# Performance work log

Measured on AMD Instinct MI355X. Metric: run time of the kernel, lower is better.

## Reference

```python
import jax, jax.numpy as jnp
import numpy as np

PAD_token, SOS_token, EOS_token = 0, 1, 2
V, E, H, B, To, Ti = 10000, 512, 512, 32, 256, 1024


def _u(key, shape, fan_in):
    s = 1.0 / np.sqrt(fan_in)
    return jax.random.uniform(key, shape, jnp.float32, -s, s)


def setup_inputs() -> dict:
    key = jax.random.key(0)
    ks = jax.random.split(key, 16)
    inp = {
        "padded_input": jax.random.randint(ks[0], (B, To), 3, V),
        "encoder_padded_outputs": jax.random.normal(ks[1], (B, Ti, H), jnp.float32),
        "embedding": jax.random.normal(ks[2], (V, E), jnp.float32) * 0.02,
        # layer 0 LSTMCell: input = embed + encoder context (E + H)
        "Wih0": _u(ks[3], (4 * H, E + H), H), "Whh0": _u(ks[4], (4 * H, H), H),
        "bih0": _u(ks[5], (4 * H,), H),       "bhh0": _u(ks[6], (4 * H,), H),
        # layer 1 LSTMCell: input = H
        "Wih1": _u(ks[7], (4 * H, H), H),     "Whh1": _u(ks[8], (4 * H, H), H),
        "bih1": _u(ks[9], (4 * H,), H),       "bhh1": _u(ks[10], (4 * H,), H),
        # MLP: Linear(2H -> H), Tanh, Linear(H -> V)
        "W1": _u(ks[11], (H, 2 * H), 2 * H),  "b1": _u(ks[12], (H,), 2 * H),
        "W2": _u(ks[13], (V, H), H),          "b2": _u(ks[14], (V,), H),
    }
    return inp


def _lstm_cell(x, h, c, Wih, Whh, bih, bhh):
    g = x @ Wih.T + bih + h @ Whh.T + bhh            # [B, 4H]
    i, f, gg, o = jnp.split(g, 4, axis=-1)           # torch gate order i,f,g,o
    c2 = jax.nn.sigmoid(f) * c + jax.nn.sigmoid(i) * jnp.tanh(gg)
    h2 = jax.nn.sigmoid(o) * jnp.tanh(c2)
    return h2, c2


def reference(padded_input, encoder_padded_outputs, embedding,
              Wih0, Whh0, bih0, bhh0, Wih1, Whh1, bih1, bhh1,
              W1, b1, W2, b2):
    n = padded_input.shape[0]
    sos = jnp.full((n, 1), SOS_token, padded_input.dtype)
    eos = jnp.full((n, 1), EOS_token, padded_input.dtype)
    ys_in = jnp.concatenate([sos, padded_input], axis=1)   # [B, To+1]
    ys_out = jnp.concatenate([padded_input, eos], axis=1)  # [B, To+1]

    emb = embedding[ys_in]                                 # [B, To+1, E]
    emb_t = jnp.swapaxes(emb, 0, 1)                        # [To+1, B, E]
    enc = encoder_padded_outputs                           # [B, Ti, H]

    h0 = jnp.zeros((n, H), enc.dtype)
    init = (h0, h0, h0, h0, jnp.zeros((n, enc.shape[2]), enc.dtype))

    def step(carry, e_t):
        h_0, c_0, h_1, c_1, att_c = carry
        rnn_in = jnp.concatenate([e_t, att_c], axis=1)
        h_0, c_0 = _lstm_cell(rnn_in, h_0, c_0, Wih0, Whh0, bih0, bhh0)
        h_1, c_1 = _lstm_cell(h_0, h_1, c_1, Wih1, Whh1, bih1, bhh1)
        scores = jnp.einsum('bh,bth->bt', h_1, enc)        # [B, Ti]
        att_w = jax.nn.softmax(scores, axis=-1)
        att_c = jnp.einsum('bt,bth->bh', att_w, enc)       # [B, H]
        mlp_in = jnp.concatenate([h_1, att_c], axis=1)
        logits = jnp.tanh(mlp_in @ W1.T + b1) @ W2.T + b2  # [B, V]
        return (h_0, c_0, h_1, c_1, att_c), logits

    _, y_all = jax.lax.scan(step, init, emb_t)             # [To+1, B, V]
    logits = jnp.swapaxes(y_all, 0, 1).reshape(-1, V)      # [B*(To+1), V]
    labels = ys_out.reshape(-1)
    logp = jax.nn.log_softmax(logits, axis=-1)
    nll = -jnp.take_along_axis(logp, labels[:, None], axis=1)[:, 0]
    mask = (labels != PAD_token).astype(logits.dtype)
    loss = jnp.sum(nll * mask) / jnp.maximum(jnp.sum(mask), 1.0)
    return loss
```

## Files before the change

### kernel.cpp

```cpp
#include <hip/hip_runtime.h>
#include <hip/hip_bf16.h>

#define B_    32
#define TO_   256
#define T_    257
#define H_    512
#define V_    10000
#define TI_   1024
#define NROW_ 8224
#define NB_   256

using f32x4 = __attribute__((ext_vector_type(4))) float;
using s16x8 = __attribute__((ext_vector_type(8))) short;

struct Ptrs {
  const int* padded;
  const float* enc;
  const float* emb;
  const float *Wih0, *Whh0, *bih0, *bhh0;
  const float *Wih1, *Whh1, *bih1, *bhh1;
  const float *W1, *b1, *W2, *b2;
  float* out;
  unsigned short *mlpin;
  unsigned short *embt;
  unsigned short *tanhv;
  unsigned short *W0c;
  unsigned short *W1c;
  unsigned short *W1b;
  unsigned short *W2b;
  float *bias0c, *bias1c;
  float *u;
  unsigned short *Xh0;
  unsigned short *Xh1;
  float *Xh1f;
  float *Zb;
  unsigned *bar;
  float *rowsum;
  float *lablog;
};

__device__ __forceinline__ unsigned short f2b(float f){
  __hip_bfloat16 h = __float2bfloat16(f);
  unsigned short r; __builtin_memcpy(&r, &h, 2); return r;
}
__device__ __forceinline__ float b2f(unsigned short u){
  unsigned v = ((unsigned)u) << 16; float f; __builtin_memcpy(&f, &v, 4); return f;
}
__device__ __forceinline__ float sigf(float x){ return 1.f / (1.f + expf(-x)); }

__device__ __forceinline__ float aldf(const float* p){
  return __hip_atomic_load(p, __ATOMIC_RELAXED, __HIP_MEMORY_SCOPE_AGENT);
}
__device__ __forceinline__ unsigned long long aldu(const unsigned long long* p){
  return __hip_atomic_load(p, __ATOMIC_RELAXED, __HIP_MEMORY_SCOPE_AGENT);
}
__device__ __forceinline__ void astf(float* p, float v){
  __hip_atomic_store(p, v, __ATOMIC_RELAXED, __HIP_MEMORY_SCOPE_AGENT);
}
__device__ __forceinline__ void astu(unsigned long long* p, unsigned long long v){
  __hip_atomic_store(p, v, __ATOMIC_RELAXED, __HIP_MEMORY_SCOPE_AGENT);
}
__device__ __forceinline__ void astw(unsigned* p, unsigned v){
  __hip_atomic_store(p, v, __ATOMIC_RELAXED, __HIP_MEMORY_SCOPE_AGENT);
}

__device__ __forceinline__ void gbar(unsigned* bar, unsigned ph){
  asm volatile("s_waitcnt vmcnt(0)" ::: "memory");
  __syncthreads();
  if (threadIdx.x == 0){
    const int g = (int)(blockIdx.x >> 5);
    unsigned a = __hip_atomic_fetch_add(bar + g * 64, 1u, __ATOMIC_RELAXED, __HIP_MEMORY_SCOPE_AGENT);
    bool done = false;
    if (a == 31u){
      unsigned r = __hip_atomic_fetch_add(bar + 512, 1u, __ATOMIC_RELAXED, __HIP_MEMORY_SCOPE_AGENT);
      if (r == 7u){
        __hip_atomic_store(bar + 512, 0u, __ATOMIC_RELAXED, __HIP_MEMORY_SCOPE_AGENT);
        #pragma unroll
        for (int i = 0; i < 8; ++i)
          __hip_atomic_store(bar + i * 64, 0u, __ATOMIC_RELAXED, __HIP_MEMORY_SCOPE_AGENT);
        asm volatile("s_waitcnt vmcnt(0)" ::: "memory");
        #pragma unroll
        for (int i = 0; i < 8; ++i)
          __hip_atomic_store(bar + (16 + i) * 64, ph, __ATOMIC_RELAXED, __HIP_MEMORY_SCOPE_AGENT);
        done = true;
      }
    }
    if (!done){
      while (__hip_atomic_load(bar + (16 + g) * 64, __ATOMIC_RELAXED, __HIP_MEMORY_SCOPE_AGENT) != ph)
        __builtin_amdgcn_s_sleep(2);
    }
  }
  __syncthreads();
}

__global__ __launch_bounds__(256) void kprep(Ptrs P){
  const int stride = gridDim.x * blockDim.x;
  const int i0 = blockIdx.x * blockDim.x + threadIdx.x;
  for (int i = i0; i < 2048; i += stride) P.bar[i] = 0u;
  for (int i = i0; i < T_ * B_ * 512; i += stride){
    int k = i & 511, tb = i >> 9, b = tb & 31, t = tb >> 5;
    int tok = (t == 0) ? 1 : P.padded[b * TO_ + (t - 1)];
    P.embt[i] = f2b(P.emb[(size_t)tok * 512 + k]);
  }
  for (int i = i0; i < 2048 * 1536; i += stride){
    int k = i % 1536, gp = i / 1536;
    int j = gp >> 2, q = gp & 3, g = q * 512 + j;
    float v = (k < 1024) ? P.Wih0[(size_t)g * 1024 + k] : P.Whh0[(size_t)g * 512 + (k - 1024)];
    P.W0c[i] = f2b(v);
  }
  for (int i = i0; i < 2048 * 1024; i += stride){
    int k = i & 1023, gp = i >> 10;
    int j = gp >> 2, q = gp & 3, g = q * 512 + j;
    float v = (k < 512) ? P.Wih1[(size_t)g * 512 + k] : P.Whh1[(size_t)g * 512 + (k - 512)];
    P.W1c[i] = f2b(v);
  }
  for (int i = i0; i < 2048; i += stride){
    int j = i >> 2, q = i & 3, g = q * 512 + j;
    P.bias0c[i] = P.bih0[g] + P.bhh0[g];
    P.bias1c[i] = P.bih1[g] + P.bhh1[g];
  }
  for (int i = i0; i < 512 * 1024; i += stride) P.W1b[i] = f2b(P.W1[i]);
  for (int i = i0; i < NROW_; i += stride) P.rowsum[i] = 0.f;
}

__global__ __launch_bounds__(256) void kprep2(Ptrs P){
  const int stride = gridDim.x * blockDim.x;
  const int i0 = blockIdx.x * blockDim.x + threadIdx.x;
  for (int i = i0; i < V_ * 512; i += stride) P.W2b[i] = f2b(P.W2[i]);
}

__global__ __launch_bounds__(256, 1) void kA(Ptrs P){
  __shared__ __align__(16) unsigned short enc_s[128 * 512];
  __shared__ float h1_s[512];
  __shared__ float w_s[128];
  __shared__ float gate_s[32][17];
  __shared__ float h_s[32][4];
  const int bb = blockIdx.x, tid = threadIdx.x;
  const int b_att = bb >> 3;
  unsigned ph = 0;

  {
    const float* ep = P.enc + ((size_t)b_att * TI_ + (size_t)(bb & 7) * 128) * H_;
    for (int idx = tid; idx < 128 * 512; idx += 256){
      int r = idx >> 9;
      unsigned byteoff = ((unsigned)idx * 2u) ^ ((unsigned)(r & 7) << 4);
      enc_s[byteoff >> 1] = f2b(ep[idx]);
    }
  }
  {
    int g = bb * 256 + tid;
    if (g < 32768){ astf(P.u + g, 0.f); astf(P.Xh1f + g, 0.f); }
    if (g < 16384){ astw((unsigned*)P.Xh0 + g, 0u); astw((unsigned*)P.Xh1 + g, 0u); }
    if (g < 64) astf(P.Zb + g, (g >= 32) ? 1.f : 0.f);
  }
  gbar(P.bar, ++ph);

  const int wv = tid >> 6;
  const int l  = tid & 63, lr = l & 15, lk = l >> 4;
  const int eidx = tid - 128;
  const int eb = eidx >> 2, ejl = eidx & 3;
  float c0r = 0.f, c1r = 0.f;

  for (int t = 0; t < T_; ++t){
    const int p = t & 1, pp = p ^ 1;
    if (bb < 128){
      if (wv < 2){
        const int batch = wv * 16 + lr;
        const unsigned short* Brow = P.W0c + (size_t)(bb * 16 + lr) * 1536;
        const unsigned short* Erow = P.embt + ((size_t)t * 32 + batch) * 512;
        const float* Urow = P.u + pp * 16384 + batch * 512;
        const unsigned long long* Hrow =
            (const unsigned long long*)(P.Xh0 + pp * 16384 + batch * 512);
        const float rZ = 1.f / aldf(P.Zb + pp * 32 + batch);
        f32x4 acc = {0.f, 0.f, 0.f, 0.f};
        #pragma unroll
        for (int ks = 0; ks < 16; ++ks){
          s16x8 a = *(const s16x8*)(Erow + ks * 32 + lk * 8);
          s16x8 b = *(const s16x8*)(Brow + ks * 32 + lk * 8);
          acc = __builtin_amdgcn_mfma_f32_16x16x32_bf16(a, b, acc, 0, 0, 0);
        }
        #pragma unroll
        for (int ks = 0; ks < 16; ++ks){
          const int kb = ks * 32 + lk * 8;
          unsigned long long dd[4];
          dd[0] = aldu((const unsigned long long*)(Urow + kb));
          dd[1] = aldu((const unsigned long long*)(Urow + kb + 2));
          dd[2] = aldu((const unsigned long long*)(Urow + kb + 4));
          dd[3] = aldu((const unsigned long long*)(Urow + kb + 6));
          float uf[8]; __builtin_memcpy(uf, dd, 32);
          s16x8 a;
          #pragma unroll
          for (int e = 0; e < 8; ++e) a[e] = (short)f2b(uf[e] * rZ);
          s16x8 b = *(const s16x8*)(Brow + 512 + kb);
          acc = __builtin_amdgcn_mfma_f32_16x16x32_bf16(a, b, acc, 0, 0, 0);
        }
        #pragma unroll
        for (int ks = 0; ks < 16; ++ks){
          const int kb = ks * 32 + lk * 8;
          unsigned long long dd[2];
          dd[0] = aldu(Hrow + (kb >> 2));
          dd[1] = aldu(Hrow + (kb >> 2) + 1);
          s16x8 a; __builtin_memcpy(&a, dd, 16);
          s16x8 b = *(const s16x8*)(Brow + 1024 + kb);
          acc = __builtin_amdgcn_mfma_f32_16x16x32_bf16(a, b, acc, 0, 0, 0);
        }
        #pragma unroll
        for (int j = 0; j < 4; ++j) gate_s[wv * 16 + lk * 4 + j][lr] = acc[j];
      }
    } else if (bb < 160 && t > 0){
      const int b = bb - 128;
      const float rZ = 1.f / aldf(P.Zb + pp * 32 + b);
      unsigned long long v = aldu((const unsigned long long*)(P.u + pp * 16384 + b * 512) + tid);
      float f2[2]; __builtin_memcpy(f2, &v, 8);
      unsigned pk = (unsigned)f2b(f2[0] * rZ) | ((unsigned)f2b(f2[1] * rZ) << 16);
      *(unsigned*)(P.mlpin + ((size_t)(t - 1) * 32 + b) * 1024 + 512 + tid * 2) = pk;
    }
    __syncthreads();
    if (bb < 128 && tid >= 128){
      const float* bs = P.bias0c + bb * 16 + ejl * 4;
      float ii = sigf (gate_s[eb][ejl * 4 + 0] + bs[0]);
      float ff = sigf (gate_s[eb][ejl * 4 + 1] + bs[1]);
      float gg = tanhf(gate_s[eb][ejl * 4 + 2] + bs[2]);
      float oo = sigf (gate_s[eb][ejl * 4 + 3] + bs[3]);
      float cn = ff * c0r + ii * gg; c0r = cn;
      h_s[eb][ejl] = oo * tanhf(cn);
    }
    __syncthreads();
    if (bb < 128 && tid < 32){
      unsigned short hb[4];
      #pragma unroll
      for (int jl = 0; jl < 4; ++jl) hb[jl] = f2b(h_s[tid][jl]);
      unsigned long long v; __builtin_memcpy(&v, hb, 8);
      astu((unsigned long long*)(P.Xh0 + p * 16384 + tid * 512 + bb * 4), v);
    }
    gbar(P.bar, ++ph);
    if (bb < 128){
      if (wv < 2){
        const int batch = wv * 16 + lr;
        const unsigned short* Brow = P.W1c + (size_t)(bb * 16 + lr) * 1024;
        const unsigned long long* H0r =
            (const unsigned long long*)(P.Xh0 + p * 16384 + batch * 512);
        const unsigned long long* H1r =
            (const unsigned long long*)(P.Xh1 + pp * 16384 + batch * 512);
        f32x4 acc = {0.f, 0.f, 0.f, 0.f};
        #pragma unroll
        for (int ks = 0; ks < 16; ++ks){
          const int kb = ks * 32 + lk * 8;
          unsigned long long dd[2];
          dd[0] = aldu(H0r + (kb >> 2));
          dd[1] = aldu(H0r + (kb >> 2) + 1);
          s16x8 a; __builtin_memcpy(&a, dd, 16);
          s16x8 b = *(const s16x8*)(Brow + kb);
          acc = __builtin_amdgcn_mfma_f32_16x16x32_bf16(a, b, acc, 0, 0, 0);
        }
        #pragma unroll
        for (int ks = 0; ks < 16; ++ks){
          const int kb = ks * 32 + lk * 8;
          unsigned long long dd[2];
          dd[0] = aldu(H1r + (kb >> 2));
          dd[1] = aldu(H1r + (kb >> 2) + 1);
          s16x8 a; __builtin_memcpy(&a, dd, 16);
          s16x8 b = *(const s16x8*)(Brow + 512 + kb);
          acc = __builtin_amdgcn_mfma_f32_16x16x32_bf16(a, b, acc, 0, 0, 0);
        }
        #pragma unroll
        for (int j = 0; j < 4; ++j) gate_s[wv * 16 + lk * 4 + j][lr] = acc[j];
      }
    } else if (bb < 224){
      astf(P.u + pp * 16384 + (bb - 160) * 256 + tid, 0.f);
    } else if (bb == 224 && tid < 32){
      astf(P.Zb + pp * 32 + tid, 0.f);
    }
    __syncthreads();
    if (bb < 128 && tid >= 128){
      const float* bs = P.bias1c + bb * 16 + ejl * 4;
      float ii = sigf (gate_s[eb][ejl * 4 + 0] + bs[0]);
      float ff = sigf (gate_s[eb][ejl * 4 + 1] + bs[1]);
      float gg = tanhf(gate_s[eb][ejl * 4 + 2] + bs[2]);
      float oo = sigf (gate_s[eb][ejl * 4 + 3] + bs[3]);
      float cn = ff * c1r + ii * gg; c1r = cn;
      h_s[eb][ejl] = oo * tanhf(cn);
    }
    __syncthreads();
    if (bb < 128 && tid < 32){
      unsigned short hb[4];
      #pragma unroll
      for (int jl = 0; jl < 4; ++jl) hb[jl] = f2b(h_s[tid][jl]);
      unsigned long long vb; __builtin_memcpy(&vb, hb, 8);
      astu((unsigned long long*)(P.Xh1 + p * 16384 + tid * 512 + bb * 4), vb);
      *(unsigned long long*)(P.mlpin + ((size_t)t * 32 + tid) * 1024 + bb * 4) = vb;
      unsigned long long w0, w1;
      __builtin_memcpy(&w0, &h_s[tid][0], 8);
      __builtin_memcpy(&w1, &h_s[tid][2], 8);
      unsigned long long* dst = (unsigned long long*)P.Xh1f + ((p * 16384 + tid * 512 + bb * 4) >> 1);
      astu(dst, w0); astu(dst + 1, w1);
    }
    gbar(P.bar, ++ph);
    {
      unsigned long long v = aldu((const unsigned long long*)(P.Xh1f + p * 16384 + b_att * 512) + tid);
      float f2[2]; __builtin_memcpy(f2, &v, 8);
      h1_s[tid * 2] = f2[0]; h1_s[tid * 2 + 1] = f2[1];
    }
    __syncthreads();
    {
      const int ti_l = tid >> 1, half = tid & 1;
      float s = 0.f;
      const unsigned swz = (unsigned)(ti_l & 7) << 4;
      for (int h8 = half * 256; h8 < half * 256 + 256; h8 += 8){
        unsigned byteoff = ((unsigned)(ti_l * 512 + h8) * 2u) ^ swz;
        s16x8 ev = *(const s16x8*)((const char*)enc_s + byteoff);
        #pragma unroll
        for (int e = 0; e < 8; ++e) s += b2f((unsigned short)ev[e]) * h1_s[h8 + e];
      }
      s += __shfl_xor(s, 1);
      if (half == 0) w_s[ti_l] = expf(s);
    }
    __syncthreads();
    {
      if (tid < 128){
        float z = w_s[tid];
        #pragma unroll
        for (int off = 1; off < 64; off <<= 1) z += __shfl_xor(z, off);
        if ((tid & 63) == 0) unsafeAtomicAdd(P.Zb + p * 32 + b_att, z);
      }
      float a0 = 0.f, a1 = 0.f;
      const int hc = tid * 2;
      for (int ti = 0; ti < 128; ++ti){
        const float wvv = w_s[ti];
        unsigned byteoff = ((unsigned)(ti * 1024 + hc * 2)) ^ ((unsigned)(ti & 7) << 4);
        unsigned pk = *(const unsigned*)((const char*)enc_s + byteoff);
        a0 += wvv * b2f((unsigned short)(pk & 0xffffu));
        a1 += wvv * b2f((unsigned short)(pk >> 16));
      }
      unsafeAtomicAdd(P.u + p * 16384 + b_att * 512 + hc, a0);
      unsafeAtomicAdd(P.u + p * 16384 + b_att * 512 + hc + 1, a1);
    }
    gbar(P.bar, ++ph);
  }
  if (bb >= 128 && bb < 160){
    const int b = bb - 128;
    const float rZ = 1.f / aldf(P.Zb + 0 * 32 + b);
    unsigned long long v = aldu((const unsigned long long*)(P.u + 0 * 16384 + b * 512) + tid);
    float f2[2]; __builtin_memcpy(f2, &v, 8);
    unsigned pk = (unsigned)f2b(f2[0] * rZ) | ((unsigned)f2b(f2[1] * rZ) << 16);
    *(unsigned*)(P.mlpin + ((size_t)256 * 32 + b) * 1024 + 512 + tid * 2) = pk;
  }
}

__global__ __launch_bounds__(256) void kB1(Ptrs P){
  const int wid = blockIdx.x * 4 + (threadIdx.x >> 6);
  if (wid >= 129 * 8) return;
  const int mt = wid >> 3, nt = wid & 7;
  const int l = threadIdx.x & 63, lr = l & 15, lk = l >> 4;
  const int mr = mt * 64, nc = nt * 64;
  f32x4 acc[4][4] = {};
  for (int k0 = 0; k0 < 1024; k0 += 32){
    s16x8 af[4], bfm[4];
    #pragma unroll
    for (int f = 0; f < 4; ++f){
      int row = mr + f * 16 + lr; if (row > NROW_ - 1) row = NROW_ - 1;
      af[f] = *(const s16x8*)(P.mlpin + (size_t)row * 1024 + k0 + lk * 8);
      int col = nc + f * 16 + lr;
      bfm[f] = *(const s16x8*)(P.W1b + (size_t)col * 1024 + k0 + lk * 8);
    }
    #pragma unroll
    for (int fi = 0; fi < 4; ++fi)
      #pragma unroll
      for (int fj = 0; fj < 4; ++fj)
        acc[fi][fj] = __builtin_amdgcn_mfma_f32_16x16x32_bf16(af[fi], bfm[fj], acc[fi][fj], 0, 0, 0);
  }
  #pragma unroll
  for (int fi = 0; fi < 4; ++fi){
    #pragma unroll
    for (int jj = 0; jj < 4; ++jj){
      int m = mr + fi * 16 + lk * 4 + jj;
      if (m >= NROW_) continue;
      #pragma unroll
      for (int fj = 0; fj < 4; ++fj){
        int n = nc + fj * 16 + lr;
        P.tanhv[(size_t)m * 512 + n] = f2b(tanhf(acc[fi][fj][jj] + P.b1[n]));
      }
    }
  }
}

__global__ __launch_bounds__(256) void kB2(Ptrs P){
  const int wid = blockIdx.x * 4 + (threadIdx.x >> 6);
  if (wid >= 129 * 157) return;
  const int mt = wid / 157, nt = wid % 157;
  const int l = threadIdx.x & 63, lr = l & 15, lk = l >> 4;
  const int mr = mt * 64, nc = nt * 64;
  f32x4 acc[4][4] = {};
  for (int k0 = 0; k0 < 512; k0 += 32){
    s16x8 af[4], bfm[4];
    #pragma unroll
    for (int f = 0; f < 4; ++f){
      int row = mr + f * 16 + lr; if (row > NROW_ - 1) row = NROW_ - 1;
      af[f] = *(const s16x8*)(P.tanhv + (size_t)row * 512 + k0 + lk * 8);
      int col = nc + f * 16 + lr; if (col > V_ - 1) col = V_ - 1;
      bfm[f] = *(const s16x8*)(P.W2b + (size_t)col * 512 + k0 + lk * 8);
    }
    #pragma unroll
    for (int fi = 0; fi < 4; ++fi)
      #pragma unroll
      for (int fj = 0; fj < 4; ++fj)
        acc[fi][fj] = __builtin_amdgcn_mfma_f32_16x16x32_bf16(af[fi], bfm[fj], acc[fi][fj], 0, 0, 0);
  }
  #pragma unroll
  for (int fi = 0; fi < 4; ++fi){
    #pragma unroll
    for (int jj = 0; jj < 4; ++jj){
      const int m = mr + fi * 16 + lk * 4 + jj;
      float s = 0.f;
      #pragma unroll
      for (int fj = 0; fj < 4; ++fj){
        int n = nc + fj * 16 + lr;
        if (n < V_) s += expf(acc[fi][fj][jj] + P.b2[n]);
      }
      s += __shfl_xor(s, 1); s += __shfl_xor(s, 2);
      s += __shfl_xor(s, 4); s += __shfl_xor(s, 8);
      if (lr == 0 && m < NROW_) unsafeAtomicAdd(P.rowsum + m, s);
    }
  }
}

__global__ __launch_bounds__(256) void kL1(Ptrs P){
  const int wid = blockIdx.x * 4 + (threadIdx.x >> 6);
  if (wid >= NROW_) return;
  const int l = threadIdx.x & 63;
  const int t = wid >> 5, b = wid & 31;
  const int lab = (t < TO_) ? P.padded[b * TO_ + t] : 2;
  float s = 0.f;
  s16x8 av = *(const s16x8*)(P.tanhv + (size_t)wid * 512 + l * 8);
  s16x8 wv = *(const s16x8*)(P.W2b + (size_t)lab * 512 + l * 8);
  #pragma unroll
  for (int e = 0; e < 8; ++e) s += b2f((unsigned short)av[e]) * b2f((unsigned short)wv[e]);
  #pragma unroll
  for (int off = 1; off < 64; off <<= 1) s += __shfl_xor(s, off);
  if (l == 0) P.lablog[wid] = s + P.b2[lab];
}

__global__ __launch_bounds__(512) void kL2(Ptrs P){
  __shared__ float ssum[8], scnt[8];
  const int tid = threadIdx.x;
  float sum = 0.f, cnt = 0.f;
  for (int r = tid; r < NROW_; r += 512){
    int t = r >> 5, b = r & 31;
    int lab = (t < TO_) ? P.padded[b * TO_ + t] : 2;
    if (lab != 0){ sum += logf(P.rowsum[r]) - P.lablog[r]; cnt += 1.f; }
  }
  #pragma unroll
  for (int off = 1; off < 64; off <<= 1){ sum += __shfl_xor(sum, off); cnt += __shfl_xor(cnt, off); }
  if ((tid & 63) == 0){ ssum[tid >> 6] = sum; scnt[tid >> 6] = cnt; }
  __syncthreads();
  if (tid == 0){
    float S = 0.f, C = 0.f;
    for (int i = 0; i < 8; ++i){ S += ssum[i]; C += scnt[i]; }
    P.out[0] = S / fmaxf(C, 1.f);
  }
}

extern "C" void kernel_launch(void* const* d_in, const int* in_sizes, int n_in,
                              void* d_out, int out_size, void* d_ws, size_t ws_size,
                              hipStream_t stream){
  (void)in_sizes; (void)n_in; (void)out_size; (void)ws_size;
  Ptrs P;
  P.padded = (const int*)d_in[0];
  P.enc    = (const float*)d_in[1];
  P.emb    = (const float*)d_in[2];
  P.Wih0 = (const float*)d_in[3];  P.Whh0 = (const float*)d_in[4];
  P.bih0 = (const float*)d_in[5];  P.bhh0 = (const float*)d_in[6];
  P.Wih1 = (const float*)d_in[7];  P.Whh1 = (const float*)d_in[8];
  P.bih1 = (const float*)d_in[9];  P.bhh1 = (const float*)d_in[10];
  P.W1 = (const float*)d_in[11];   P.b1 = (const float*)d_in[12];
  P.W2 = (const float*)d_in[13];   P.b2 = (const float*)d_in[14];
  P.out = (float*)d_out;

  char* w = (char*)d_ws;
  size_t off = 0;
  auto take = [&](size_t bytes) -> void* {
    void* ptr = (void*)(w + off);
    off += (bytes + 255) & ~(size_t)255;
    return ptr;
  };
  P.mlpin  = (unsigned short*)take((size_t)T_ * B_ * 1024 * 2);
  P.embt   = (unsigned short*)take((size_t)T_ * B_ * 512 * 2);
  P.tanhv  = P.embt;
  P.W0c    = (unsigned short*)take((size_t)2048 * 1536 * 2);
  P.W1c    = (unsigned short*)take((size_t)2048 * 1024 * 2);
  P.W2b    = P.W0c;
  P.W1b    = (unsigned short*)take((size_t)512 * 1024 * 2);
  P.bias0c = (float*)take(2048 * 4);
  P.bias1c = (float*)take(2048 * 4);
  P.u      = (float*)take(2 * 32 * 512 * 4);
  P.Xh0    = (unsigned short*)take(2 * 32 * 512 * 2);
  P.Xh1    = (unsigned short*)take(2 * 32 * 512 * 2);
  P.Xh1f   = (float*)take(2 * 32 * 512 * 4);
  P.Zb     = (float*)take(2 * 32 * 4);
  P.bar    = (unsigned*)take(8192);
  P.rowsum = (float*)take(NROW_ * 4);
  P.lablog = (float*)take(NROW_ * 4);

  kprep<<<dim3(2048), dim3(256), 0, stream>>>(P);
  void* args[] = { (void*)&P };
  hipLaunchCooperativeKernel(kA, dim3(NB_), dim3(256), args, 0, stream);
  kprep2<<<dim3(1024), dim3(256), 0, stream>>>(P);
  kB1<<<dim3(258),  dim3(256), 0, stream>>>(P);
  kB2<<<dim3(5064), dim3(256), 0, stream>>>(P);
  kL1<<<dim3(2056), dim3(256), 0, stream>>>(P);
  kL2<<<dim3(1),    dim3(512), 0, stream>>>(P);
}
```

Measured before the change: 9.490 ms.

## Replace atomic-counter grid barrier with per-block flag barrier and partial layer barrier

The hierarchical fetch-add grid barrier is replaced by a flag barrier. Each block publishes a monotonically increasing phase value to its own slot, and one wave polls all slots with a wave-wide vote. The barrier between LSTM layer 0 and layer 1 now covers only the 128 recurrent blocks, and the zeroing of the attention accumulators moves into the first phase, so the other blocks skip that synchronization. The aim is to cut per-step barrier latency across the 257 sequential steps, at the cost of more polling loads per barrier and more reliance on ordering subtleties between the phases.

```diff
diff --git a/kernel.cpp b/kernel.cpp
--- a/kernel.cpp
+++ b/kernel.cpp
@@ -51,6 +51,9 @@
 __device__ __forceinline__ float aldf(const float* p){
   return __hip_atomic_load(p, __ATOMIC_RELAXED, __HIP_MEMORY_SCOPE_AGENT);
 }
+__device__ __forceinline__ unsigned aldw(const unsigned* p){
+  return __hip_atomic_load(p, __ATOMIC_RELAXED, __HIP_MEMORY_SCOPE_AGENT);
+}
 __device__ __forceinline__ unsigned long long aldu(const unsigned long long* p){
   return __hip_atomic_load(p, __ATOMIC_RELAXED, __HIP_MEMORY_SCOPE_AGENT);
 }
@@ -67,27 +70,34 @@
 __device__ __forceinline__ void gbar(unsigned* bar, unsigned ph){
   asm volatile("s_waitcnt vmcnt(0)" ::: "memory");
   __syncthreads();
-  if (threadIdx.x == 0){
-    const int g = (int)(blockIdx.x >> 5);
-    unsigned a = __hip_atomic_fetch_add(bar + g * 64, 1u, __ATOMIC_RELAXED, __HIP_MEMORY_SCOPE_AGENT);
-    bool done = false;
-    if (a == 31u){
-      unsigned r = __hip_atomic_fetch_add(bar + 512, 1u, __ATOMIC_RELAXED, __HIP_MEMORY_SCOPE_AGENT);
-      if (r == 7u){
-        __hip_atomic_store(bar + 512, 0u, __ATOMIC_RELAXED, __HIP_MEMORY_SCOPE_AGENT);
-        #pragma unroll
-        for (int i = 0; i < 8; ++i)
-          __hip_atomic_store(bar + i * 64, 0u, __ATOMIC_RELAXED, __HIP_MEMORY_SCOPE_AGENT);
-        asm volatile("s_waitcnt vmcnt(0)" ::: "memory");
-        #pragma unroll
-        for (int i = 0; i < 8; ++i)
-          __hip_atomic_store(bar + (16 + i) * 64, ph, __ATOMIC_RELAXED, __HIP_MEMORY_SCOPE_AGENT);
-        done = true;
-      }
-    }
-    if (!done){
-      while (__hip_atomic_load(bar + (16 + g) * 64, __ATOMIC_RELAXED, __HIP_MEMORY_SCOPE_AGENT) != ph)
-        __builtin_amdgcn_s_sleep(2);
+  if (threadIdx.x < 64){
+    const int l = threadIdx.x;
+    if (l == 0) astw(bar + blockIdx.x * 4, ph);
+    for (;;){
+      unsigned f0 = aldw(bar + (l      ) * 4);
+      unsigned f1 = aldw(bar + (l +  64) * 4);
+      unsigned f2 = aldw(bar + (l + 128) * 4);
+      unsigned f3 = aldw(bar + (l + 192) * 4);
+      bool ok = (f0 >= ph) & (f1 >= ph) & (f2 >= ph) & (f3 >= ph);
+      if (__all(ok)) break;
+      __builtin_amdgcn_s_sleep(2);
+    }
+  }
+  __syncthreads();
+}
+
+__device__ __forceinline__ void gbar128(unsigned* bar, unsigned ph){
+  asm volatile("s_waitcnt vmcnt(0)" ::: "memory");
+  __syncthreads();
+  if (threadIdx.x < 64){
+    const int l = threadIdx.x;
+    if (l == 0) astw(bar + blockIdx.x * 4, ph);
+    for (;;){
+      unsigned f0 = aldw(bar + (l     ) * 4);
+      unsigned f1 = aldw(bar + (l + 64) * 4);
+      bool ok = (f0 >= ph) & (f1 >= ph);
+      if (__all(ok)) break;
+      __builtin_amdgcn_s_sleep(2);
     }
   }
   __syncthreads();
@@ -137,7 +147,6 @@
   __shared__ float h_s[32][4];
   const int bb = blockIdx.x, tid = threadIdx.x;
   const int b_att = bb >> 3;
-  unsigned ph = 0;
 
   {
     const float* ep = P.enc + ((size_t)b_att * TI_ + (size_t)(bb & 7) * 128) * H_;
@@ -153,7 +162,7 @@
     if (g < 16384){ astw((unsigned*)P.Xh0 + g, 0u); astw((unsigned*)P.Xh1 + g, 0u); }
     if (g < 64) astf(P.Zb + g, (g >= 32) ? 1.f : 0.f);
   }
-  gbar(P.bar, ++ph);
+  gbar(P.bar, 1u);
 
   const int wv = tid >> 6;
   const int l  = tid & 63, lr = l & 15, lk = l >> 4;
@@ -163,6 +172,7 @@
 
   for (int t = 0; t < T_; ++t){
     const int p = t & 1, pp = p ^ 1;
+    const unsigned phb = 3u * (unsigned)t;
     if (bb < 128){
       if (wv < 2){
         const int batch = wv * 16 + lr;
@@ -207,33 +217,41 @@
         #pragma unroll
         for (int j = 0; j < 4; ++j) gate_s[wv * 16 + lk * 4 + j][lr] = acc[j];
       }
-    } else if (bb < 160 && t > 0){
-      const int b = bb - 128;
-      const float rZ = 1.f / aldf(P.Zb + pp * 32 + b);
-      unsigned long long v = aldu((const unsigned long long*)(P.u + pp * 16384 + b * 512) + tid);
-      float f2[2]; __builtin_memcpy(f2, &v, 8);
-      unsigned pk = (unsigned)f2b(f2[0] * rZ) | ((unsigned)f2b(f2[1] * rZ) << 16);
-      *(unsigned*)(P.mlpin + ((size_t)(t - 1) * 32 + b) * 1024 + 512 + tid * 2) = pk;
-    }
-    __syncthreads();
-    if (bb < 128 && tid >= 128){
-      const float* bs = P.bias0c + bb * 16 + ejl * 4;
-      float ii = sigf (gate_s[eb][ejl * 4 + 0] + bs[0]);
-      float ff = sigf (gate_s[eb][ejl * 4 + 1] + bs[1]);
-      float gg = tanhf(gate_s[eb][ejl * 4 + 2] + bs[2]);
-      float oo = sigf (gate_s[eb][ejl * 4 + 3] + bs[3]);
-      float cn = ff * c0r + ii * gg; c0r = cn;
-      h_s[eb][ejl] = oo * tanhf(cn);
-    }
-    __syncthreads();
-    if (bb < 128 && tid < 32){
-      unsigned short hb[4];
-      #pragma unroll
-      for (int jl = 0; jl < 4; ++jl) hb[jl] = f2b(h_s[tid][jl]);
-      unsigned long long v; __builtin_memcpy(&v, hb, 8);
-      astu((unsigned long long*)(P.Xh0 + p * 16384 + tid * 512 + bb * 4), v);
-    }
-    gbar(P.bar, ++ph);
+    } else if (bb < 160){
+      if (t > 0){
+        const int b = bb - 128;
+        const float rZ = 1.f / aldf(P.Zb + pp * 32 + b);
+        unsigned long long v = aldu((const unsigned long long*)(P.u + pp * 16384 + b * 512) + tid);
+        float f2[2]; __builtin_memcpy(f2, &v, 8);
+        unsigned pk = (unsigned)f2b(f2[0] * rZ) | ((unsigned)f2b(f2[1] * rZ) << 16);
+        *(unsigned*)(P.mlpin + ((size_t)(t - 1) * 32 + b) * 1024 + 512 + tid * 2) = pk;
+      }
+    } else if (bb < 224){
+      astf(P.u + p * 16384 + (bb - 160) * 256 + tid, 0.f);
+    } else if (bb == 224 && tid < 32){
+      astf(P.Zb + p * 32 + tid, 0.f);
+    }
+    if (bb < 128){
+      __syncthreads();
+      if (tid >= 128){
+        const float* bs = P.bias0c + bb * 16 + ejl * 4;
+        float ii = sigf (gate_s[eb][ejl * 4 + 0] + bs[0]);
+        float ff = sigf (gate_s[eb][ejl * 4 + 1] + bs[1]);
+        float gg = tanhf(gate_s[eb][ejl * 4 + 2] + bs[2]);
+        float oo = sigf (gate_s[eb][ejl * 4 + 3] + bs[3]);
+        float cn = ff * c0r + ii * gg; c0r = cn;
+        h_s[eb][ejl] = oo * tanhf(cn);
+      }
+      __syncthreads();
+      if (tid < 32){
+        unsigned short hb[4];
+        #pragma unroll
+        for (int jl = 0; jl < 4; ++jl) hb[jl] = f2b(h_s[tid][jl]);
+        unsigned long long v; __builtin_memcpy(&v, hb, 8);
+        astu((unsigned long long*)(P.Xh0 + p * 16384 + tid * 512 + bb * 4), v);
+      }
+      gbar128(P.bar, phb + 2u);
+    }
     if (bb < 128){
       if (wv < 2){
         const int batch = wv * 16 + lr;
@@ -266,36 +284,32 @@
         #pragma unroll
         for (int j = 0; j < 4; ++j) gate_s[wv * 16 + lk * 4 + j][lr] = acc[j];
       }
-    } else if (bb < 224){
-      astf(P.u + pp * 16384 + (bb - 160) * 256 + tid, 0.f);
-    } else if (bb == 224 && tid < 32){
-      astf(P.Zb + pp * 32 + tid, 0.f);
-    }
-    __syncthreads();
-    if (bb < 128 && tid >= 128){
-      const float* bs = P.bias1c + bb * 16 + ejl * 4;
-      float ii = sigf (gate_s[eb][ejl * 4 + 0] + bs[0]);
-      float ff = sigf (gate_s[eb][ejl * 4 + 1] + bs[1]);
-      float gg = tanhf(gate_s[eb][ejl * 4 + 2] + bs[2]);
-      float oo = sigf (gate_s[eb][ejl * 4 + 3] + bs[3]);
-      float cn = ff * c1r + ii * gg; c1r = cn;
-      h_s[eb][ejl] = oo * tanhf(cn);
-    }
-    __syncthreads();
-    if (bb < 128 && tid < 32){
-      unsigned short hb[4];
-      #pragma unroll
-      for (int jl = 0; jl < 4; ++jl) hb[jl] = f2b(h_s[tid][jl]);
-      unsigned long long vb; __builtin_memcpy(&vb, hb, 8);
-      astu((unsigned long long*)(P.Xh1 + p * 16384 + tid * 512 + bb * 4), vb);
-      *(unsigned long long*)(P.mlpin + ((size_t)t * 32 + tid) * 1024 + bb * 4) = vb;
-      unsigned long long w0, w1;
-      __builtin_memcpy(&w0, &h_s[tid][0], 8);
-      __builtin_memcpy(&w1, &h_s[tid][2], 8);
-      unsigned long long* dst = (unsigned long long*)P.Xh1f + ((p * 16384 + tid * 512 + bb * 4) >> 1);
-      astu(dst, w0); astu(dst + 1, w1);
-    }
-    gbar(P.bar, ++ph);
+      __syncthreads();
+      if (tid >= 128){
+        const float* bs = P.bias1c + bb * 16 + ejl * 4;
+        float ii = sigf (gate_s[eb][ejl * 4 + 0] + bs[0]);
+        float ff = sigf (gate_s[eb][ejl * 4 + 1] + bs[1]);
+        float gg = tanhf(gate_s[eb][ejl * 4 + 2] + bs[2]);
+        float oo = sigf (gate_s[eb][ejl * 4 + 3] + bs[3]);
+        float cn = ff * c1r + ii * gg; c1r = cn;
+        h_s[eb][ejl] = oo * tanhf(cn);
+      }
+      __syncthreads();
+      if (tid < 32){
+        unsigned short hb[4];
+        #pragma unroll
+        for (int jl = 0; jl < 4; ++jl) hb[jl] = f2b(h_s[tid][jl]);
+        unsigned long long vb; __builtin_memcpy(&vb, hb, 8);
+        astu((unsigned long long*)(P.Xh1 + p * 16384 + tid * 512 + bb * 4), vb);
+        *(unsigned long long*)(P.mlpin + ((size_t)t * 32 + tid) * 1024 + bb * 4) = vb;
+        unsigned long long w0, w1;
+        __builtin_memcpy(&w0, &h_s[tid][0], 8);
+        __builtin_memcpy(&w1, &h_s[tid][2], 8);
+        unsigned long long* dst = (unsigned long long*)P.Xh1f + ((p * 16384 + tid * 512 + bb * 4) >> 1);
+        astu(dst, w0); astu(dst + 1, w1);
+      }
+    }
+    gbar(P.bar, phb + 3u);
     {
       unsigned long long v = aldu((const unsigned long long*)(P.Xh1f + p * 16384 + b_att * 512) + tid);
       float f2[2]; __builtin_memcpy(f2, &v, 8);
@@ -335,7 +349,7 @@
       unsafeAtomicAdd(P.u + p * 16384 + b_att * 512 + hc, a0);
       unsafeAtomicAdd(P.u + p * 16384 + b_att * 512 + hc + 1, a1);
     }
-    gbar(P.bar, ++ph);
+    gbar(P.bar, phb + 4u);
   }
   if (bb >= 128 && bb < 160){
     const int b = bb - 128;
```

After: 9.451 ms. No clear change (-0.4%).
